# Optimization experiments

Measured on AMD Instinct MI355X. Metric: run time of the kernel, lower is better.

The kernel has to match this reference:

```python
import jax, jax.numpy as jnp
import numpy as np
import math

N = 100_000   # nodes
E = 1_600_000 # edges (avg degree 16)
IN = 128      # in_channels
H, C = 4, 32  # heads, out_channels (H*C = 128)
ED = 16       # edge_dim


def setup_inputs() -> dict:
    key = jax.random.key(0)
    ks = jax.random.split(key, 12)
    s = 0.02
    return {
        "x": jax.random.normal(ks[0], (N, IN), jnp.float32),
        "edge_attr": jax.random.normal(ks[1], (E, ED), jnp.float32),
        "edge_index": jax.random.randint(ks[2], (2, E), 0, N, dtype=jnp.int32),
        "Wq": jax.random.normal(ks[3], (IN, H * C), jnp.float32) * s,
        "bq": jnp.zeros((H * C,), jnp.float32),
        "Wk": jax.random.normal(ks[4], (IN, H * C), jnp.float32) * s,
        "bk": jnp.zeros((H * C,), jnp.float32),
        "Wv": jax.random.normal(ks[5], (IN, H * C), jnp.float32) * s,
        "bv": jnp.zeros((H * C,), jnp.float32),
        "We": jax.random.normal(ks[6], (ED, H * C), jnp.float32) * s,
        "Wskip": jax.random.normal(ks[7], (IN, H * C), jnp.float32) * s,
        "bskip": jnp.zeros((H * C,), jnp.float32),
        "Wbeta": jax.random.normal(ks[8], (3 * H * C, 1), jnp.float32) * s,
    }


def reference(x, edge_attr, edge_index, Wq, bq, Wk, bk, Wv, bv, We, Wskip, bskip, Wbeta):
    n = x.shape[0]
    q = (x @ Wq + bq).reshape(n, H, C)
    k = (x @ Wk + bk).reshape(n, H, C)
    v = (x @ Wv + bv).reshape(n, H, C)

    row, col = edge_index[0], edge_index[1]  # dst (target), src (source)

    # per-edge attention logits, with edge-feature fusion into keys
    k_j = k[col] + (edge_attr @ We).reshape(-1, H, C)   # [E, H, C]
    alpha = jnp.einsum("ehc,ehc->eh", q[row], k_j) / math.sqrt(C)  # [E, H]

    # scatter softmax over each destination node's neighborhood.
    # Original code stabilizes by subtracting a per-group constant via a
    m = jnp.zeros((n, H), alpha.dtype).at[row].set(alpha)  # per-group constant
    ex = jnp.exp(alpha - m[row])                            # [E, H]
    denom = jax.ops.segment_sum(ex, row, num_segments=n)    # [N, H]
    alpha = ex / (denom[row] + 1e-16)

    # weighted scatter-add aggregation of values
    msgs = v[col] * alpha[..., None]                        # [E, H, C]
    out = jax.ops.segment_sum(msgs, row, num_segments=n)    # [N, H, C]
    out = out.reshape(n, H * C)                             # concat heads

    # gated skip connection (root_weight + beta)
    x_skip = x @ Wskip + bskip                              # [N, H*C]
    beta = jax.nn.sigmoid(
        jnp.concatenate([out, x_skip, out - x_skip], axis=-1) @ Wbeta
    )                                                       # [N, 1]
    return beta * x_skip + (1.0 - beta) * out
```

## Files before the change

### kernel.cpp

```cpp
#include <hip/hip_runtime.h>
#include <stdint.h>

typedef unsigned int uint;
typedef unsigned short ushort;

typedef __attribute__((ext_vector_type(8))) short bf16x8;
typedef __attribute__((ext_vector_type(16))) float f32x16;
typedef __attribute__((ext_vector_type(4))) int   i32x4;
typedef __attribute__((ext_vector_type(4))) float f32x4;

__device__ inline float bflo(uint u) {
    union { uint x; float f; } z; z.x = u << 16; return z.f;
}
__device__ inline float bfhi(uint u) {
    union { uint x; float f; } z; z.x = u & 0xffff0000u; return z.f;
}
__device__ inline ushort f2bf(float f) {
    union { float f; uint u; } x; x.f = f;
    uint r = (x.u + 0x7fffu + ((x.u >> 16) & 1u)) >> 16;
    return (ushort)r;
}

__global__ __launch_bounds__(256) void pack_x(const float* __restrict__ x,
                                              uint4* __restrict__ xfrag,
                                              int n, int nchunks)
{
    int o = blockIdx.x * 256 + threadIdx.x;
    if (o >= nchunks) return;
    int m    = o & 127;
    int kb   = (o >> 7) & 15;
    int tile = o >> 11;
    int row  = tile * 128 + m;
    float4 lo = make_float4(0.f, 0.f, 0.f, 0.f);
    float4 hi = make_float4(0.f, 0.f, 0.f, 0.f);
    if (row < n) {
        lo = *(const float4*)&x[(size_t)row * 128 + kb * 8];
        hi = *(const float4*)&x[(size_t)row * 128 + kb * 8 + 4];
    }
    uint4 ov;
    ov.x = (uint)f2bf(lo.x) | ((uint)f2bf(lo.y) << 16);
    ov.y = (uint)f2bf(lo.z) | ((uint)f2bf(lo.w) << 16);
    ov.z = (uint)f2bf(hi.x) | ((uint)f2bf(hi.y) << 16);
    ov.w = (uint)f2bf(hi.z) | ((uint)f2bf(hi.w) << 16);
    xfrag[o] = ov;
}

__global__ __launch_bounds__(256) void pack_w(
    const float* __restrict__ W0, const float* __restrict__ W1,
    const float* __restrict__ W2, const float* __restrict__ W3,
    uint4* __restrict__ wfrag)
{
    int o = blockIdx.x * 256 + threadIdx.x;
    if (o >= 8192) return;
    int nn = o & 127;
    int kb = (o >> 7) & 15;
    int j  = o >> 11;
    const float* W = (j == 0) ? W0 : (j == 1) ? W1 : (j == 2) ? W2 : W3;
    float v[8];
    #pragma unroll
    for (int i = 0; i < 8; ++i) v[i] = W[(size_t)(kb * 8 + i) * 128 + nn];
    uint4 ov;
    ov.x = (uint)f2bf(v[0]) | ((uint)f2bf(v[1]) << 16);
    ov.y = (uint)f2bf(v[2]) | ((uint)f2bf(v[3]) << 16);
    ov.z = (uint)f2bf(v[4]) | ((uint)f2bf(v[5]) << 16);
    ov.w = (uint)f2bf(v[6]) | ((uint)f2bf(v[7]) << 16);
    wfrag[o] = ov;
}

__global__ __launch_bounds__(256) void lin_mfma(
    const uint4* __restrict__ xfrag, const uint4* __restrict__ wfrag,
    const float* __restrict__ bq, const float* __restrict__ bk,
    const float* __restrict__ bv, const float* __restrict__ bs,
    uint* __restrict__ qout, uint* __restrict__ kvout, uint* __restrict__ sout,
    int n)
{
    const int tile = blockIdx.x;
    const int w  = threadIdx.x >> 6;
    const int l  = threadIdx.x & 63;
    const int lm = l & 31, lh = l >> 5;

    bf16x8 a[8];
    const uint4* ap = xfrag + (size_t)tile * 2048 + lh * 128 + w * 32 + lm;
    #pragma unroll
    for (int ks = 0; ks < 8; ++ks) a[ks] = *(const bf16x8*)(ap + ks * 256);

    const int rowbase = tile * 128 + w * 32 + 4 * lh;

    #pragma unroll
    for (int j = 0; j < 4; ++j) {
        const float* bias = (j == 0) ? bq : (j == 1) ? bk : (j == 2) ? bv : bs;
        uint* dst; int stride, cbase;
        if (j == 0)      { dst = qout;  stride = 64;  cbase = 0;  }
        else if (j == 1) { dst = kvout; stride = 128; cbase = 0;  }
        else if (j == 2) { dst = kvout; stride = 128; cbase = 64; }
        else             { dst = sout;  stride = 64;  cbase = 0;  }

        #pragma unroll
        for (int np = 0; np < 2; ++np) {
            const uint4* bp0 = wfrag + (size_t)j * 2048 + lh * 128 + (np * 2) * 32 + lm;
            f32x16 c0, c1;
            #pragma unroll
            for (int i = 0; i < 16; ++i) { c0[i] = 0.f; c1[i] = 0.f; }
            #pragma unroll
            for (int ks = 0; ks < 8; ++ks) {
                bf16x8 B0 = *(const bf16x8*)(bp0 + ks * 256);
                bf16x8 B1 = *(const bf16x8*)(bp0 + 32 + ks * 256);
                c0 = __builtin_amdgcn_mfma_f32_32x32x16_bf16(a[ks], B0, c0, 0, 0, 0);
                c1 = __builtin_amdgcn_mfma_f32_32x32x16_bf16(a[ks], B1, c1, 0, 0, 0);
            }
            #pragma unroll
            for (int t = 0; t < 2; ++t) {
                f32x16 cc = t ? c1 : c0;
                int gc = (np * 2 + t) * 32 + lm;
                float bl = bias[gc];
                #pragma unroll
                for (int r = 0; r < 16; ++r) {
                    float val = cc[r] + bl;
                    float partner = __shfl_xor(val, 1);
                    int gr = rowbase + (r & 3) + 8 * (r >> 2);
                    if (!(lm & 1) && gr < n) {
                        uint pk = (uint)f2bf(val) | ((uint)f2bf(partner) << 16);
                        dst[(size_t)gr * stride + cbase + (gc >> 1)] = pk;
                    }
                }
            }
        }
    }
}

__global__ __launch_bounds__(256) void t_kernel(const uint* __restrict__ qb,
                                                const float* __restrict__ We,
                                                uint* __restrict__ tb, int n)
{
    int wid = (blockIdx.x * blockDim.x + threadIdx.x) >> 6;
    int lane = threadIdx.x & 63;
    if (wid >= n) return;
    int h = lane >> 4, d = lane & 15;
    const uint* qp = qb + (size_t)wid * 64 + h * 16;
    const float* wp = We + (size_t)d * 128 + h * 32;
    float s = 0.f;
    #pragma unroll
    for (int j4 = 0; j4 < 16; j4 += 4) {
        uint4 u = *(const uint4*)(qp + j4);
        float4 wA = *(const float4*)&wp[2 * j4];
        float4 wB = *(const float4*)&wp[2 * j4 + 4];
        s += bflo(u.x) * wA.x + bfhi(u.x) * wA.y
           + bflo(u.y) * wA.z + bfhi(u.y) * wA.w
           + bflo(u.z) * wB.x + bfhi(u.z) * wB.y
           + bflo(u.w) * wB.z + bfhi(u.w) * wB.w;
    }
    float partner = __shfl_xor(s, 1);
    if (!(lane & 1)) {
        uint pk = (uint)f2bf(s) | ((uint)f2bf(partner) << 16);
        tb[(size_t)wid * 32 + (lane >> 1)] = pk;
    }
}

__global__ void hist_kernel(const int* __restrict__ rows, int* __restrict__ counts,
                            int* __restrict__ rank, int e)
{
    int i = blockIdx.x * blockDim.x + threadIdx.x;
    if (i < e) rank[i] = atomicAdd(&counts[rows[i]], 1);
}

__global__ __launch_bounds__(1024) void scan1_kernel(int* __restrict__ data,
                                                     int* __restrict__ bsum, int n)
{
    __shared__ int s[1024];
    int i = blockIdx.x * 1024 + threadIdx.x;
    int v = (i < n) ? data[i] : 0;
    s[threadIdx.x] = v;
    __syncthreads();
    for (int offd = 1; offd < 1024; offd <<= 1) {
        int add = (threadIdx.x >= offd) ? s[threadIdx.x - offd] : 0;
        __syncthreads();
        s[threadIdx.x] += add;
        __syncthreads();
    }
    if (i < n) data[i] = s[threadIdx.x];
    if (threadIdx.x == 1023) bsum[blockIdx.x] = s[1023];
}

__global__ __launch_bounds__(1024) void scan2_kernel(const int* __restrict__ bsum,
                                                     int* __restrict__ bofs, int nb)
{
    __shared__ int s[1024];
    int tid = threadIdx.x;
    int v = (tid < nb) ? bsum[tid] : 0;
    s[tid] = v;
    __syncthreads();
    for (int o = 1; o < 1024; o <<= 1) {
        int add = (tid >= o) ? s[tid - o] : 0;
        __syncthreads();
        s[tid] += add;
        __syncthreads();
    }
    if (tid < nb) bofs[tid] = s[tid] - v;
}

__global__ __launch_bounds__(1024) void scan3_kernel(const int* __restrict__ incl,
                                                     const int* __restrict__ bofs,
                                                     int* __restrict__ offsets, int n)
{
    int i = blockIdx.x * 1024 + threadIdx.x;
    if (i == 0) offsets[0] = 0;
    if (i < n) offsets[i + 1] = incl[i] + bofs[blockIdx.x];
}

__global__ __launch_bounds__(256) void scatter_g_kernel(
    const int* __restrict__ rows, const int* __restrict__ cols,
    const float* __restrict__ ea, const uint* __restrict__ tb,
    const int* __restrict__ offsets, const int* __restrict__ rank,
    i32x4* __restrict__ csr, int e)
{
    int i = blockIdx.x * blockDim.x + threadIdx.x;
    if (i >= e) return;
    int r  = rows[i];
    int rk = rank[i];
    int c  = cols[i];
    int pos = offsets[r] + rk;

    const f32x4* ep = (const f32x4*)&ea[(size_t)i * 16];
    f32x4 e0 = __builtin_nontemporal_load(ep);
    f32x4 e1 = __builtin_nontemporal_load(ep + 1);
    f32x4 e2 = __builtin_nontemporal_load(ep + 2);
    f32x4 e3 = __builtin_nontemporal_load(ep + 3);
    const uint* tp = tb + (size_t)r * 32;
    float g[4];
    #pragma unroll
    for (int h = 0; h < 4; ++h) {
        uint4 ua = *(const uint4*)(tp + h * 8);
        uint4 ub = *(const uint4*)(tp + h * 8 + 4);
        g[h] = e0[0] * bflo(ua.x) + e0[1] * bfhi(ua.x)
             + e0[2] * bflo(ua.y) + e0[3] * bfhi(ua.y)
             + e1[0] * bflo(ua.z) + e1[1] * bfhi(ua.z)
             + e1[2] * bflo(ua.w) + e1[3] * bfhi(ua.w)
             + e2[0] * bflo(ub.x) + e2[1] * bfhi(ub.x)
             + e2[2] * bflo(ub.y) + e2[3] * bfhi(ub.y)
             + e3[0] * bflo(ub.z) + e3[1] * bfhi(ub.z)
             + e3[2] * bflo(ub.w) + e3[3] * bfhi(ub.w);
    }
    i32x4 rec;
    rec.x = c;
    rec.y = 0;
    rec.z = (int)((uint)f2bf(g[0]) | ((uint)f2bf(g[1]) << 16));
    rec.w = (int)((uint)f2bf(g[2]) | ((uint)f2bf(g[3]) << 16));
    csr[pos] = rec;
}

__global__ __launch_bounds__(256) void agg_kernel(
    const uint* __restrict__ qb, const uint* __restrict__ kv,
    const uint* __restrict__ sb, const i32x4* __restrict__ csr,
    const int* __restrict__ offsets, const float* __restrict__ Wbeta,
    float* __restrict__ out, int n)
{
    int wid = (blockIdx.x * blockDim.x + threadIdx.x) >> 6;
    int lane = threadIdx.x & 63;
    if (wid >= n) return;
    const int es = lane >> 4;
    const int h  = (lane >> 2) & 3;
    const int cq = lane & 3;
    const int c0 = h * 32 + cq * 8;

    uint4 uq = *(const uint4*)&qb[(size_t)wid * 64 + h * 16 + cq * 4];
    float qv[8] = { bflo(uq.x), bfhi(uq.x), bflo(uq.y), bfhi(uq.y),
                    bflo(uq.z), bfhi(uq.z), bflo(uq.w), bfhi(uq.w) };

    const int beg = offsets[wid], end = offsets[wid + 1];
    const float scale = 0.17677669529663687f;

    float denom = 0.f;
    float acc[8];
    #pragma unroll
    for (int j = 0; j < 8; ++j) acc[j] = 0.f;

    for (int i = beg; i < end; i += 4) {
        int idx = i + es;
        bool valid = idx < end;
        int cidx = valid ? idx : end - 1;
        i32x4 se = __builtin_nontemporal_load(&csr[cidx]);
        uint gp = (h & 2) ? (uint)se.w : (uint)se.z;
        float gh = (h & 1) ? bfhi(gp) : bflo(gp);
        const uint* krow = kv + (size_t)se.x * 128 + h * 16 + cq * 4;
        uint4 kp = *(const uint4*)krow;
        uint4 vp = *(const uint4*)(krow + 64);

        float part = qv[0] * bflo(kp.x) + qv[1] * bfhi(kp.x)
                   + qv[2] * bflo(kp.y) + qv[3] * bfhi(kp.y)
                   + qv[4] * bflo(kp.z) + qv[5] * bfhi(kp.z)
                   + qv[6] * bflo(kp.w) + qv[7] * bfhi(kp.w);
        part += __shfl_xor(part, 1);
        part += __shfl_xor(part, 2);
        float p = valid ? __expf((part + gh) * scale) : 0.f;
        denom += p;
        acc[0] += p * bflo(vp.x); acc[1] += p * bfhi(vp.x);
        acc[2] += p * bflo(vp.y); acc[3] += p * bfhi(vp.y);
        acc[4] += p * bflo(vp.z); acc[5] += p * bfhi(vp.z);
        acc[6] += p * bflo(vp.w); acc[7] += p * bfhi(vp.w);
    }

    denom += __shfl_xor(denom, 16);
    denom += __shfl_xor(denom, 32);
    #pragma unroll
    for (int j = 0; j < 8; ++j) {
        acc[j] += __shfl_xor(acc[j], 16);
        acc[j] += __shfl_xor(acc[j], 32);
    }

    float inv = 1.f / (denom + 1e-16f);
    float o[8];
    #pragma unroll
    for (int j = 0; j < 8; ++j) o[j] = acc[j] * inv;

    uint4 us = *(const uint4*)&sb[(size_t)wid * 64 + h * 16 + cq * 4];
    float xsv[8] = { bflo(us.x), bfhi(us.x), bflo(us.y), bfhi(us.y),
                     bflo(us.z), bfhi(us.z), bflo(us.w), bfhi(us.w) };

    float bp = 0.f;
    #pragma unroll
    for (int j = 0; j < 8; ++j) {
        bp += o[j]   * Wbeta[c0 + j]
            + xsv[j] * Wbeta[128 + c0 + j]
            + (o[j] - xsv[j]) * Wbeta[256 + c0 + j];
    }
    bp += __shfl_xor(bp, 1);
    bp += __shfl_xor(bp, 2);
    bp += __shfl_xor(bp, 4);
    bp += __shfl_xor(bp, 8);
    float beta = 1.f / (1.f + __expf(-bp));

    if (es == 0) {
        float r[8];
        #pragma unroll
        for (int j = 0; j < 8; ++j) r[j] = beta * xsv[j] + (1.f - beta) * o[j];
        f32x4 r0 = { r[0], r[1], r[2], r[3] };
        f32x4 r1 = { r[4], r[5], r[6], r[7] };
        __builtin_nontemporal_store(r0, (f32x4*)&out[(size_t)wid * 128 + c0]);
        __builtin_nontemporal_store(r1, (f32x4*)&out[(size_t)wid * 128 + c0 + 4]);
    }
}

extern "C" void kernel_launch(void* const* d_in, const int* in_sizes, int n_in,
                              void* d_out, int out_size, void* d_ws, size_t ws_size,
                              hipStream_t stream)
{
    const float* x     = (const float*)d_in[0];
    const float* ea    = (const float*)d_in[1];
    const int*   ei    = (const int*)d_in[2];
    const float* Wq    = (const float*)d_in[3];
    const float* bq    = (const float*)d_in[4];
    const float* Wk    = (const float*)d_in[5];
    const float* bk    = (const float*)d_in[6];
    const float* Wv    = (const float*)d_in[7];
    const float* bv    = (const float*)d_in[8];
    const float* We    = (const float*)d_in[9];
    const float* Wsk   = (const float*)d_in[10];
    const float* bsk   = (const float*)d_in[11];
    const float* Wbeta = (const float*)d_in[12];
    float* out = (float*)d_out;

    const int N = in_sizes[0] / 128;
    const int E = in_sizes[1] / 16;
    const int NT = (N + 127) / 128;
    const int nchunks = NT * 2048;

    char* base = (char*)d_ws;
    size_t off = 0;
    auto alloc = [&](size_t bytes) -> void* {
        void* p = base + off;
        off += (bytes + 255) & ~(size_t)255;
        return p;
    };
    int*    tmp     = (int*)alloc((size_t)N * 4);
    int*    offsets = (int*)alloc((size_t)(N + 1) * 4);
    int*    bsum    = (int*)alloc(4096 * 4);
    int*    bofs    = (int*)alloc(4096 * 4);
    int*    rank    = (int*)alloc((size_t)E * 4);
    size_t  xfrag_bytes = (size_t)nchunks * 16;
    size_t  csr_bytes   = (size_t)E * 16;
    char*   shared_reg  = (char*)alloc(xfrag_bytes > csr_bytes ? xfrag_bytes : csr_bytes);
    uint4*  xfrag   = (uint4*)shared_reg;
    i32x4*  csr     = (i32x4*)shared_reg;
    uint4*  wfrag   = (uint4*)alloc((size_t)8192 * 16);
    uint*   qbuf    = (uint*)alloc((size_t)N * 64 * 4);
    uint*   sbuf    = (uint*)alloc((size_t)N * 64 * 4);
    uint*   tbuf    = (uint*)alloc((size_t)N * 32 * 4);
    uint*   kvbuf   = (uint*)alloc((size_t)N * 128 * 4);
    (void)ws_size; (void)n_in; (void)out_size;

    hipMemsetAsync(tmp, 0, (size_t)N * 4, stream);

    pack_x<<<(nchunks + 255) / 256, 256, 0, stream>>>(x, xfrag, N, nchunks);
    pack_w<<<32, 256, 0, stream>>>(Wq, Wk, Wv, Wsk, wfrag);
    lin_mfma<<<NT, 256, 0, stream>>>(xfrag, wfrag, bq, bk, bv, bsk,
                                     qbuf, kvbuf, sbuf, N);
    t_kernel<<<(N + 3) / 4, 256, 0, stream>>>(qbuf, We, tbuf, N);
    hist_kernel<<<(E + 255) / 256, 256, 0, stream>>>(ei, tmp, rank, E);
    int nb = (N + 1023) / 1024;
    scan1_kernel<<<nb, 1024, 0, stream>>>(tmp, bsum, N);
    scan2_kernel<<<1, 1024, 0, stream>>>(bsum, bofs, nb);
    scan3_kernel<<<nb, 1024, 0, stream>>>(tmp, bofs, offsets, N);
    scatter_g_kernel<<<(E + 255) / 256, 256, 0, stream>>>(ei, ei + E, ea, tbuf,
                                                          offsets, rank, csr, E);
    agg_kernel<<<(N + 3) / 4, 256, 0, stream>>>(qbuf, kvbuf, sbuf, csr,
                                                offsets, Wbeta, out, N);
}
```

Baseline: 669.5 us.

## Fold q·We projection into MFMA GEMM and merge scan passes

Precomputes the combined matrix Wq·We (and bias bq·We) in pack_w, so lin_mfma gains a fifth output block that produces the per-node t vectors directly. This removes the separate t_kernel launch and its reread of q. The second and third scan kernels are merged: each block redoes the small block-sum scan itself. The CSR record store becomes nontemporal. The cost is extra MFMA work, redundant block-sum scans in every block, and slightly different rounding, because t is now computed from fp32 weights instead of bf16-rounded q.

```diff
diff --git a/kernel.cpp b/kernel.cpp
--- a/kernel.cpp
+++ b/kernel.cpp
@@ -48,17 +48,44 @@
 __global__ __launch_bounds__(256) void pack_w(
     const float* __restrict__ W0, const float* __restrict__ W1,
     const float* __restrict__ W2, const float* __restrict__ W3,
-    uint4* __restrict__ wfrag)
+    const float* __restrict__ We, const float* __restrict__ bq,
+    uint4* __restrict__ wfrag, float* __restrict__ btbuf)
 {
     int o = blockIdx.x * 256 + threadIdx.x;
-    if (o >= 8192) return;
-    int nn = o & 127;
-    int kb = (o >> 7) & 15;
-    int j  = o >> 11;
-    const float* W = (j == 0) ? W0 : (j == 1) ? W1 : (j == 2) ? W2 : W3;
+    if (o >= 10240) return;
     float v[8];
-    #pragma unroll
-    for (int i = 0; i < 8; ++i) v[i] = W[(size_t)(kb * 8 + i) * 128 + nn];
+    if (o < 8192) {
+        int nn = o & 127;
+        int kb = (o >> 7) & 15;
+        int j  = o >> 11;
+        const float* W = (j == 0) ? W0 : (j == 1) ? W1 : (j == 2) ? W2 : W3;
+        #pragma unroll
+        for (int i = 0; i < 8; ++i) v[i] = W[(size_t)(kb * 8 + i) * 128 + nn];
+    } else {
+        int o2 = o - 8192;
+        int nn = o2 & 127;
+        int kb = (o2 >> 7) & 15;
+        #pragma unroll
+        for (int i = 0; i < 8; ++i) v[i] = 0.f;
+        if (nn < 64) {
+            int h = nn >> 4, d = nn & 15;
+            const float* wq = W0 + h * 32;
+            const float* we = We + (size_t)d * 128 + h * 32;
+            #pragma unroll
+            for (int i = 0; i < 8; ++i) {
+                int k = kb * 8 + i;
+                float s = 0.f;
+                for (int c = 0; c < 32; ++c)
+                    s += wq[(size_t)k * 128 + c] * we[c];
+                v[i] = s;
+            }
+            if (kb == 0) {
+                float s = 0.f;
+                for (int c = 0; c < 32; ++c) s += bq[h * 32 + c] * we[c];
+                btbuf[nn] = s;
+            }
+        }
+    }
     uint4 ov;
     ov.x = (uint)f2bf(v[0]) | ((uint)f2bf(v[1]) << 16);
     ov.y = (uint)f2bf(v[2]) | ((uint)f2bf(v[3]) << 16);
@@ -71,8 +98,9 @@
     const uint4* __restrict__ xfrag, const uint4* __restrict__ wfrag,
     const float* __restrict__ bq, const float* __restrict__ bk,
     const float* __restrict__ bv, const float* __restrict__ bs,
+    const float* __restrict__ bt,
     uint* __restrict__ qout, uint* __restrict__ kvout, uint* __restrict__ sout,
-    int n)
+    uint* __restrict__ tout, int n)
 {
     const int tile = blockIdx.x;
     const int w  = threadIdx.x >> 6;
@@ -87,16 +115,19 @@
     const int rowbase = tile * 128 + w * 32 + 4 * lh;
 
     #pragma unroll
-    for (int j = 0; j < 4; ++j) {
-        const float* bias = (j == 0) ? bq : (j == 1) ? bk : (j == 2) ? bv : bs;
+    for (int j = 0; j < 5; ++j) {
+        const float* bias = (j == 0) ? bq : (j == 1) ? bk : (j == 2) ? bv
+                          : (j == 3) ? bs : bt;
         uint* dst; int stride, cbase;
         if (j == 0)      { dst = qout;  stride = 64;  cbase = 0;  }
         else if (j == 1) { dst = kvout; stride = 128; cbase = 0;  }
         else if (j == 2) { dst = kvout; stride = 128; cbase = 64; }
-        else             { dst = sout;  stride = 64;  cbase = 0;  }
+        else if (j == 3) { dst = sout;  stride = 64;  cbase = 0;  }
+        else             { dst = tout;  stride = 32;  cbase = 0;  }
+        const int npc = (j == 4) ? 1 : 2;
 
         #pragma unroll
-        for (int np = 0; np < 2; ++np) {
+        for (int np = 0; np < npc; ++np) {
             const uint4* bp0 = wfrag + (size_t)j * 2048 + lh * 128 + (np * 2) * 32 + lm;
             f32x16 c0, c1;
             #pragma unroll
@@ -128,34 +159,6 @@
     }
 }
 
-__global__ __launch_bounds__(256) void t_kernel(const uint* __restrict__ qb,
-                                                const float* __restrict__ We,
-                                                uint* __restrict__ tb, int n)
-{
-    int wid = (blockIdx.x * blockDim.x + threadIdx.x) >> 6;
-    int lane = threadIdx.x & 63;
-    if (wid >= n) return;
-    int h = lane >> 4, d = lane & 15;
-    const uint* qp = qb + (size_t)wid * 64 + h * 16;
-    const float* wp = We + (size_t)d * 128 + h * 32;
-    float s = 0.f;
-    #pragma unroll
-    for (int j4 = 0; j4 < 16; j4 += 4) {
-        uint4 u = *(const uint4*)(qp + j4);
-        float4 wA = *(const float4*)&wp[2 * j4];
-        float4 wB = *(const float4*)&wp[2 * j4 + 4];
-        s += bflo(u.x) * wA.x + bfhi(u.x) * wA.y
-           + bflo(u.y) * wA.z + bfhi(u.y) * wA.w
-           + bflo(u.z) * wB.x + bfhi(u.z) * wB.y
-           + bflo(u.w) * wB.z + bfhi(u.w) * wB.w;
-    }
-    float partner = __shfl_xor(s, 1);
-    if (!(lane & 1)) {
-        uint pk = (uint)f2bf(s) | ((uint)f2bf(partner) << 16);
-        tb[(size_t)wid * 32 + (lane >> 1)] = pk;
-    }
-}
-
 __global__ void hist_kernel(const int* __restrict__ rows, int* __restrict__ counts,
                             int* __restrict__ rank, int e)
 {
@@ -181,8 +184,10 @@
     if (threadIdx.x == 1023) bsum[blockIdx.x] = s[1023];
 }
 
-__global__ __launch_bounds__(1024) void scan2_kernel(const int* __restrict__ bsum,
-                                                     int* __restrict__ bofs, int nb)
+__global__ __launch_bounds__(1024) void scan23_kernel(const int* __restrict__ incl,
+                                                      const int* __restrict__ bsum,
+                                                      int* __restrict__ offsets,
+                                                      int n, int nb)
 {
     __shared__ int s[1024];
     int tid = threadIdx.x;
@@ -195,16 +200,10 @@
         s[tid] += add;
         __syncthreads();
     }
-    if (tid < nb) bofs[tid] = s[tid] - v;
-}
-
-__global__ __launch_bounds__(1024) void scan3_kernel(const int* __restrict__ incl,
-                                                     const int* __restrict__ bofs,
-                                                     int* __restrict__ offsets, int n)
-{
-    int i = blockIdx.x * 1024 + threadIdx.x;
+    int bofs = (blockIdx.x == 0) ? 0 : s[blockIdx.x - 1];
+    int i = blockIdx.x * 1024 + tid;
     if (i == 0) offsets[0] = 0;
-    if (i < n) offsets[i + 1] = incl[i] + bofs[blockIdx.x];
+    if (i < n) offsets[i + 1] = incl[i] + bofs;
 }
 
 __global__ __launch_bounds__(256) void scatter_g_kernel(
@@ -245,7 +244,7 @@
     rec.y = 0;
     rec.z = (int)((uint)f2bf(g[0]) | ((uint)f2bf(g[1]) << 16));
     rec.w = (int)((uint)f2bf(g[2]) | ((uint)f2bf(g[3]) << 16));
-    csr[pos] = rec;
+    __builtin_nontemporal_store(rec, &csr[pos]);
 }
 
 __global__ __launch_bounds__(256) void agg_kernel(
@@ -374,14 +373,14 @@
     int*    tmp     = (int*)alloc((size_t)N * 4);
     int*    offsets = (int*)alloc((size_t)(N + 1) * 4);
     int*    bsum    = (int*)alloc(4096 * 4);
-    int*    bofs    = (int*)alloc(4096 * 4);
     int*    rank    = (int*)alloc((size_t)E * 4);
+    float*  btbuf   = (float*)alloc(256);
     size_t  xfrag_bytes = (size_t)nchunks * 16;
     size_t  csr_bytes   = (size_t)E * 16;
     char*   shared_reg  = (char*)alloc(xfrag_bytes > csr_bytes ? xfrag_bytes : csr_bytes);
     uint4*  xfrag   = (uint4*)shared_reg;
     i32x4*  csr     = (i32x4*)shared_reg;
-    uint4*  wfrag   = (uint4*)alloc((size_t)8192 * 16);
+    uint4*  wfrag   = (uint4*)alloc((size_t)10240 * 16);
     uint*   qbuf    = (uint*)alloc((size_t)N * 64 * 4);
     uint*   sbuf    = (uint*)alloc((size_t)N * 64 * 4);
     uint*   tbuf    = (uint*)alloc((size_t)N * 32 * 4);
@@ -391,15 +390,13 @@
     hipMemsetAsync(tmp, 0, (size_t)N * 4, stream);
 
     pack_x<<<(nchunks + 255) / 256, 256, 0, stream>>>(x, xfrag, N, nchunks);
-    pack_w<<<32, 256, 0, stream>>>(Wq, Wk, Wv, Wsk, wfrag);
-    lin_mfma<<<NT, 256, 0, stream>>>(xfrag, wfrag, bq, bk, bv, bsk,
-                                     qbuf, kvbuf, sbuf, N);
-    t_kernel<<<(N + 3) / 4, 256, 0, stream>>>(qbuf, We, tbuf, N);
+    pack_w<<<40, 256, 0, stream>>>(Wq, Wk, Wv, Wsk, We, bq, wfrag, btbuf);
+    lin_mfma<<<NT, 256, 0, stream>>>(xfrag, wfrag, bq, bk, bv, bsk, btbuf,
+                                     qbuf, kvbuf, sbuf, tbuf, N);
     hist_kernel<<<(E + 255) / 256, 256, 0, stream>>>(ei, tmp, rank, E);
     int nb = (N + 1023) / 1024;
     scan1_kernel<<<nb, 1024, 0, stream>>>(tmp, bsum, N);
-    scan2_kernel<<<1, 1024, 0, stream>>>(bsum, bofs, nb);
-    scan3_kernel<<<nb, 1024, 0, stream>>>(tmp, bofs, offsets, N);
+    scan23_kernel<<<nb, 1024, 0, stream>>>(tmp, bsum, offsets, N, nb);
     scatter_g_kernel<<<(E + 255) / 256, 256, 0, stream>>>(ei, ei + E, ea, tbuf,
                                                           offsets, rank, csr, E);
     agg_kernel<<<(N + 3) / 4, 256, 0, stream>>>(qbuf, kvbuf, sbuf, csr,
```

Result: faster. 594.2 us (-11.3%).
